# Optimization experiments

Measured on AMD Instinct MI355X. Metric: run time of the kernel, lower is better.

The kernel has to match this reference:

```python
import jax, jax.numpy as jnp
import numpy as np

T_STEPS, BATCH, DH, L = 256, 128, 512, 3  # L=3 is the only shape-consistent conv length (kernel=3, no pad)


def _conv3(x, W, b):
    # Conv1d(Dh->2, k=3) on a length-3 signal == full contraction over (Dh, 3)
    # x: (B, Dh, 3), W: (2, Dh, 3), b: (2,) -> (B, 2, 1)
    out = jnp.einsum('bdl,odl->bo', x, W) + b
    return out[:, :, None]


def setup_inputs() -> dict:
    key = jax.random.key(0)
    ks = jax.random.split(key, 5)
    inputs = jax.random.normal(ks[0], (T_STEPS, BATCH, DH, L), dtype=jnp.float32)
    h0 = jnp.zeros((BATCH, DH, L), jnp.float32)
    c0 = jnp.zeros((BATCH, DH, L), jnp.float32)
    scale = 1.0 / np.sqrt(DH * L).astype(np.float32)
    Wr = jax.random.normal(ks[1], (2, DH, L), jnp.float32) * scale  # recurrent_kernel (orthogonal-ish init)
    br = jnp.full((2,), 0.5, jnp.float32)                           # recurrent bias init 0.5
    Wc = jax.random.normal(ks[2], (2, DH, L), jnp.float32) * scale  # cell_memory_kernel
    bc = jnp.zeros((2,), jnp.float32)                               # cell_memory bias init 0
    Wi = jax.random.normal(ks[3], (2, DH, L), jnp.float32) * scale  # input_kernel
    bi = jax.random.normal(ks[4], (2,), jnp.float32) * scale
    return dict(inputs=inputs, h0=h0, c0=c0, Wr=Wr, br=br, Wc=Wc, bc=bc, Wi=Wi, bi=bi)


def reference(inputs, h0, c0, Wr, br, Wc, bc, Wi, bi):
    sig = jax.nn.sigmoid  # fun_gate

    def step(state, xt):
        h, c = state  # (B, Dh, 3) each
        cm = _conv3(c, Wc, bc)
        Cc, Ch = cm[:, 0:1], cm[:, 1:2]   # (B,1,1) each (chunk(2, dim=1))
        rm = _conv3(h, Wr, br)
        Hc, Hh = rm[:, 0:1], rm[:, 1:2]
        im = _conv3(xt, Wi, bi)
        Xc, Xh = im[:, 0:1], im[:, 1:2]
        gh = (1.0 - sig(Ch)) * Xh + (1.0 - sig(Hh)) * h   # broadcast (B,1,1)*(B,Dh,3)
        gc = (1.0 - sig(Hc)) * Xc + (1.0 - sig(Cc)) * c
        ht = jnp.tanh(gh)  # fun_main
        ct = jnp.tanh(gc)
        return (ht, ct), ht

    (hT, cT), outs = jax.lax.scan(step, (h0, c0), inputs)
    return outs, hT, cT
```

## Files before the change

kernel.cpp:

```cpp
#include <hip/hip_runtime.h>

#define T_STEPS 256
#define BATCH   128
#define FEAT    1536
#define NPAIRS  (T_STEPS * BATCH)

template <int CTRL, int RMASK>
__device__ __forceinline__ float dpp_add_step(float v) {
    int m = __builtin_amdgcn_update_dpp(0, __float_as_int(v), CTRL, RMASK, 0xF, true);
    return v + __int_as_float(m);
}

__device__ __forceinline__ float wave_reduce63(float v) {
    v = dpp_add_step<0x111, 0xF>(v);
    v = dpp_add_step<0x112, 0xF>(v);
    v = dpp_add_step<0x114, 0xF>(v);
    v = dpp_add_step<0x118, 0xF>(v);
    v = dpp_add_step<0x142, 0xA>(v);
    v = dpp_add_step<0x143, 0xC>(v);
    return v;
}

__device__ __forceinline__ float one_minus_sig(float x) {
    float e = __builtin_amdgcn_exp2f(x * 1.4426950408889634f);
    return __builtin_amdgcn_rcpf(1.0f + e);
}

__device__ __forceinline__ float tanh_fast(float x) {
    float e = __builtin_amdgcn_exp2f(x * 2.8853900817779268f);
    return fmaf(-2.0f, __builtin_amdgcn_rcpf(1.0f + e), 1.0f);
}

__device__ __forceinline__ void barrier_lds_only() {
    asm volatile("s_waitcnt lgkmcnt(0)\n\ts_barrier" ::: "memory");
}

__global__ __launch_bounds__(256) void xdot_kernel(
    const float* __restrict__ x,
    const float* __restrict__ Wi,
    const float* __restrict__ bi,
    float* __restrict__ X)
{
    const int p    = blockIdx.x;
    const int tid  = threadIdx.x;
    const int wid  = tid >> 6;
    const int lane = tid & 63;

    __shared__ float red[8];

    const float* xp = x + (size_t)p * FEAT;
    const float4 v4 = ((const float4*)xp)[tid];
    const float2 v2 = ((const float2*)(xp + 1024))[tid];

    const float4 w04 = ((const float4*)Wi)[tid];
    const float2 w02 = ((const float2*)(Wi + 1024))[tid];
    const float4 w14 = ((const float4*)(Wi + FEAT))[tid];
    const float2 w12 = ((const float2*)(Wi + FEAT + 1024))[tid];

    float a0 = v4.x * w04.x + v4.y * w04.y + v4.z * w04.z + v4.w * w04.w
             + v2.x * w02.x + v2.y * w02.y;
    float a1 = v4.x * w14.x + v4.y * w14.y + v4.z * w14.z + v4.w * w14.w
             + v2.x * w12.x + v2.y * w12.y;

    a0 = wave_reduce63(a0);
    a1 = wave_reduce63(a1);
    if (lane == 63) {
        red[wid * 2]     = a0;
        red[wid * 2 + 1] = a1;
    }
    __syncthreads();
    if (tid == 0) {
        const float s0 = red[0] + red[2] + red[4] + red[6] + bi[0];
        const float s1 = red[1] + red[3] + red[5] + red[7] + bi[1];
        const int b = p & (BATCH - 1);
        const int t = p >> 7;
        ((float2*)X)[b * T_STEPS + t] = make_float2(s0, s1);
    }
}

__global__ __launch_bounds__(256) void scan_kernel(
    const float* __restrict__ h0,
    const float* __restrict__ c0,
    const float* __restrict__ Wr, const float* __restrict__ br,
    const float* __restrict__ Wc, const float* __restrict__ bc,
    const float* __restrict__ X,
    float* __restrict__ outs,
    float* __restrict__ hT,
    float* __restrict__ cT)
{
    const int b    = blockIdx.x;
    const int tid  = threadIdx.x;
    const int wid  = tid >> 6;
    const int lane = tid & 63;

    __shared__ float4 red[2][4];
    __shared__ float2 Xsh[T_STEPS];

    Xsh[tid] = ((const float2*)X)[b * T_STEPS + tid];

    const float4 wr0_4 = ((const float4*)Wr)[tid];
    const float4 wr1_4 = ((const float4*)(Wr + FEAT))[tid];
    const float2 wr0_2 = ((const float2*)(Wr + 1024))[tid];
    const float2 wr1_2 = ((const float2*)(Wr + FEAT + 1024))[tid];
    const float4 wc0_4 = ((const float4*)Wc)[tid];
    const float4 wc1_4 = ((const float4*)(Wc + FEAT))[tid];
    const float2 wc0_2 = ((const float2*)(Wc + 1024))[tid];
    const float2 wc1_2 = ((const float2*)(Wc + FEAT + 1024))[tid];
    const float br0 = br[0], br1 = br[1];
    const float bc0 = bc[0], bc1 = bc[1];

    const float* h0b = h0 + (size_t)b * FEAT;
    const float* c0b = c0 + (size_t)b * FEAT;
    float4 h4 = ((const float4*)h0b)[tid];
    float2 h2 = ((const float2*)(h0b + 1024))[tid];
    float4 c4 = ((const float4*)c0b)[tid];
    float2 c2 = ((const float2*)(c0b + 1024))[tid];

    float* op = outs + (size_t)b * FEAT;
    const size_t OSTRIDE = (size_t)BATCH * FEAT;

    __syncthreads();

    auto step = [&](float4* buf, int t) {
        const float2 Xv = Xsh[t];

        float pHc = h4.x * wr0_4.x + h4.y * wr0_4.y + h4.z * wr0_4.z + h4.w * wr0_4.w
                  + h2.x * wr0_2.x + h2.y * wr0_2.y;
        float pHh = h4.x * wr1_4.x + h4.y * wr1_4.y + h4.z * wr1_4.z + h4.w * wr1_4.w
                  + h2.x * wr1_2.x + h2.y * wr1_2.y;
        float pCc = c4.x * wc0_4.x + c4.y * wc0_4.y + c4.z * wc0_4.z + c4.w * wc0_4.w
                  + c2.x * wc0_2.x + c2.y * wc0_2.y;
        float pCh = c4.x * wc1_4.x + c4.y * wc1_4.y + c4.z * wc1_4.z + c4.w * wc1_4.w
                  + c2.x * wc1_2.x + c2.y * wc1_2.y;

        pHc = wave_reduce63(pHc);
        pHh = wave_reduce63(pHh);
        pCc = wave_reduce63(pCc);
        pCh = wave_reduce63(pCh);

        if (lane == 63) {
            buf[wid] = make_float4(pHc, pHh, pCc, pCh);
        }
        barrier_lds_only();
        const float4 r0 = buf[0];
        const float4 r1 = buf[1];
        const float4 r2 = buf[2];
        const float4 r3 = buf[3];
        const float Hc = r0.x + r1.x + r2.x + r3.x + br0;
        const float Hh = r0.y + r1.y + r2.y + r3.y + br1;
        const float Cc = r0.z + r1.z + r2.z + r3.z + bc0;
        const float Ch = r0.w + r1.w + r2.w + r3.w + bc1;

        const float Ah = one_minus_sig(Ch) * Xv.y;
        const float Sh = one_minus_sig(Hh);
        const float Ac = one_minus_sig(Hc) * Xv.x;
        const float Sc = one_minus_sig(Cc);

        h4.x = tanh_fast(fmaf(Sh, h4.x, Ah));
        h4.y = tanh_fast(fmaf(Sh, h4.y, Ah));
        h4.z = tanh_fast(fmaf(Sh, h4.z, Ah));
        h4.w = tanh_fast(fmaf(Sh, h4.w, Ah));
        h2.x = tanh_fast(fmaf(Sh, h2.x, Ah));
        h2.y = tanh_fast(fmaf(Sh, h2.y, Ah));

        c4.x = tanh_fast(fmaf(Sc, c4.x, Ac));
        c4.y = tanh_fast(fmaf(Sc, c4.y, Ac));
        c4.z = tanh_fast(fmaf(Sc, c4.z, Ac));
        c4.w = tanh_fast(fmaf(Sc, c4.w, Ac));
        c2.x = tanh_fast(fmaf(Sc, c2.x, Ac));
        c2.y = tanh_fast(fmaf(Sc, c2.y, Ac));

        ((float4*)op)[tid]          = h4;
        ((float2*)(op + 1024))[tid] = h2;
        op += OSTRIDE;
    };

#pragma unroll 1
    for (int t = 0; t < T_STEPS; t += 2) {
        step(red[0], t);
        step(red[1], t + 1);
    }

    float* hp = hT + (size_t)b * FEAT;
    ((float4*)hp)[tid]          = h4;
    ((float2*)(hp + 1024))[tid] = h2;
    float* cp = cT + (size_t)b * FEAT;
    ((float4*)cp)[tid]          = c4;
    ((float2*)(cp + 1024))[tid] = c2;
}

extern "C" void kernel_launch(void* const* d_in, const int* in_sizes, int n_in,
                              void* d_out, int out_size, void* d_ws, size_t ws_size,
                              hipStream_t stream) {
    const float* inputs = (const float*)d_in[0];
    const float* h0     = (const float*)d_in[1];
    const float* c0     = (const float*)d_in[2];
    const float* Wr     = (const float*)d_in[3];
    const float* br     = (const float*)d_in[4];
    const float* Wc     = (const float*)d_in[5];
    const float* bc     = (const float*)d_in[6];
    const float* Wi     = (const float*)d_in[7];
    const float* bi     = (const float*)d_in[8];

    float* out = (float*)d_out;
    float* X   = (float*)d_ws;

    float* outs = out;
    float* hT   = out + (size_t)NPAIRS * FEAT;
    float* cT   = hT + (size_t)BATCH * FEAT;

    xdot_kernel<<<NPAIRS, 256, 0, stream>>>(inputs, Wi, bi, X);
    scan_kernel<<<BATCH, 256, 0, stream>>>(h0, c0, Wr, br, Wc, bc, X,
                                           outs, hT, cT);
}
```

Baseline: 449.8 us.

## Fuse input projection into scan kernel with two-step-ahead input prefetch

Measured after the change: 442.2 us. About the same (-1.7%).

```diff
diff --git a/kernel.cpp b/kernel.cpp
--- a/kernel.cpp
+++ b/kernel.cpp
@@ -35,55 +35,13 @@
     asm volatile("s_waitcnt lgkmcnt(0)\n\ts_barrier" ::: "memory");
 }
 
-__global__ __launch_bounds__(256) void xdot_kernel(
-    const float* __restrict__ x,
-    const float* __restrict__ Wi,
-    const float* __restrict__ bi,
-    float* __restrict__ X)
-{
-    const int p    = blockIdx.x;
-    const int tid  = threadIdx.x;
-    const int wid  = tid >> 6;
-    const int lane = tid & 63;
-
-    __shared__ float red[8];
-
-    const float* xp = x + (size_t)p * FEAT;
-    const float4 v4 = ((const float4*)xp)[tid];
-    const float2 v2 = ((const float2*)(xp + 1024))[tid];
-
-    const float4 w04 = ((const float4*)Wi)[tid];
-    const float2 w02 = ((const float2*)(Wi + 1024))[tid];
-    const float4 w14 = ((const float4*)(Wi + FEAT))[tid];
-    const float2 w12 = ((const float2*)(Wi + FEAT + 1024))[tid];
-
-    float a0 = v4.x * w04.x + v4.y * w04.y + v4.z * w04.z + v4.w * w04.w
-             + v2.x * w02.x + v2.y * w02.y;
-    float a1 = v4.x * w14.x + v4.y * w14.y + v4.z * w14.z + v4.w * w14.w
-             + v2.x * w12.x + v2.y * w12.y;
-
-    a0 = wave_reduce63(a0);
-    a1 = wave_reduce63(a1);
-    if (lane == 63) {
-        red[wid * 2]     = a0;
-        red[wid * 2 + 1] = a1;
-    }
-    __syncthreads();
-    if (tid == 0) {
-        const float s0 = red[0] + red[2] + red[4] + red[6] + bi[0];
-        const float s1 = red[1] + red[3] + red[5] + red[7] + bi[1];
-        const int b = p & (BATCH - 1);
-        const int t = p >> 7;
-        ((float2*)X)[b * T_STEPS + t] = make_float2(s0, s1);
-    }
-}
-
-__global__ __launch_bounds__(256) void scan_kernel(
+__global__ __launch_bounds__(256) void scan_fused_kernel(
+    const float* __restrict__ inputs,
     const float* __restrict__ h0,
     const float* __restrict__ c0,
     const float* __restrict__ Wr, const float* __restrict__ br,
     const float* __restrict__ Wc, const float* __restrict__ bc,
-    const float* __restrict__ X,
+    const float* __restrict__ Wi, const float* __restrict__ bi,
     float* __restrict__ outs,
     float* __restrict__ hT,
     float* __restrict__ cT)
@@ -93,10 +51,8 @@
     const int wid  = tid >> 6;
     const int lane = tid & 63;
 
-    __shared__ float4 red[2][4];
-    __shared__ float2 Xsh[T_STEPS];
-
-    Xsh[tid] = ((const float2*)X)[b * T_STEPS + tid];
+    __shared__ float4 red4[2][4];
+    __shared__ float2 red2[2][4];
 
     const float4 wr0_4 = ((const float4*)Wr)[tid];
     const float4 wr1_4 = ((const float4*)(Wr + FEAT))[tid];
@@ -106,8 +62,13 @@
     const float4 wc1_4 = ((const float4*)(Wc + FEAT))[tid];
     const float2 wc0_2 = ((const float2*)(Wc + 1024))[tid];
     const float2 wc1_2 = ((const float2*)(Wc + FEAT + 1024))[tid];
+    const float4 wi0_4 = ((const float4*)Wi)[tid];
+    const float4 wi1_4 = ((const float4*)(Wi + FEAT))[tid];
+    const float2 wi0_2 = ((const float2*)(Wi + 1024))[tid];
+    const float2 wi1_2 = ((const float2*)(Wi + FEAT + 1024))[tid];
     const float br0 = br[0], br1 = br[1];
     const float bc0 = bc[0], bc1 = bc[1];
+    const float bi0 = bi[0], bi1 = bi[1];
 
     const float* h0b = h0 + (size_t)b * FEAT;
     const float* c0b = c0 + (size_t)b * FEAT;
@@ -116,14 +77,18 @@
     float4 c4 = ((const float4*)c0b)[tid];
     float2 c2 = ((const float2*)(c0b + 1024))[tid];
 
+    const float*  xbase   = inputs + (size_t)b * FEAT;
+    const size_t  XSTRIDE = (size_t)BATCH * FEAT;
+
+    float4 xa4 = ((const float4*)xbase)[tid];
+    float2 xa2 = ((const float2*)(xbase + 1024))[tid];
+    float4 xb4 = ((const float4*)(xbase + XSTRIDE))[tid];
+    float2 xb2 = ((const float2*)(xbase + XSTRIDE + 1024))[tid];
+
     float* op = outs + (size_t)b * FEAT;
     const size_t OSTRIDE = (size_t)BATCH * FEAT;
 
-    __syncthreads();
-
-    auto step = [&](float4* buf, int t) {
-        const float2 Xv = Xsh[t];
-
+    auto step = [&](float4* buf4, float2* buf2, int t, float4& x4, float2& x2) {
         float pHc = h4.x * wr0_4.x + h4.y * wr0_4.y + h4.z * wr0_4.z + h4.w * wr0_4.w
                   + h2.x * wr0_2.x + h2.y * wr0_2.y;
         float pHh = h4.x * wr1_4.x + h4.y * wr1_4.y + h4.z * wr1_4.z + h4.w * wr1_4.w
@@ -132,28 +97,48 @@
                   + c2.x * wc0_2.x + c2.y * wc0_2.y;
         float pCh = c4.x * wc1_4.x + c4.y * wc1_4.y + c4.z * wc1_4.z + c4.w * wc1_4.w
                   + c2.x * wc1_2.x + c2.y * wc1_2.y;
+        float pXc = x4.x * wi0_4.x + x4.y * wi0_4.y + x4.z * wi0_4.z + x4.w * wi0_4.w
+                  + x2.x * wi0_2.x + x2.y * wi0_2.y;
+        float pXh = x4.x * wi1_4.x + x4.y * wi1_4.y + x4.z * wi1_4.z + x4.w * wi1_4.w
+                  + x2.x * wi1_2.x + x2.y * wi1_2.y;
+
+        {
+            const int tn = (t + 2 < T_STEPS) ? (t + 2) : (T_STEPS - 1);
+            const float* xp = xbase + (size_t)tn * XSTRIDE;
+            x4 = ((const float4*)xp)[tid];
+            x2 = ((const float2*)(xp + 1024))[tid];
+        }
 
         pHc = wave_reduce63(pHc);
         pHh = wave_reduce63(pHh);
         pCc = wave_reduce63(pCc);
         pCh = wave_reduce63(pCh);
+        pXc = wave_reduce63(pXc);
+        pXh = wave_reduce63(pXh);
 
         if (lane == 63) {
-            buf[wid] = make_float4(pHc, pHh, pCc, pCh);
+            buf4[wid] = make_float4(pHc, pHh, pCc, pCh);
+            buf2[wid] = make_float2(pXc, pXh);
         }
         barrier_lds_only();
-        const float4 r0 = buf[0];
-        const float4 r1 = buf[1];
-        const float4 r2 = buf[2];
-        const float4 r3 = buf[3];
+        const float4 r0 = buf4[0];
+        const float4 r1 = buf4[1];
+        const float4 r2 = buf4[2];
+        const float4 r3 = buf4[3];
+        const float2 s0 = buf2[0];
+        const float2 s1 = buf2[1];
+        const float2 s2 = buf2[2];
+        const float2 s3 = buf2[3];
         const float Hc = r0.x + r1.x + r2.x + r3.x + br0;
         const float Hh = r0.y + r1.y + r2.y + r3.y + br1;
         const float Cc = r0.z + r1.z + r2.z + r3.z + bc0;
         const float Ch = r0.w + r1.w + r2.w + r3.w + bc1;
+        const float Xc = s0.x + s1.x + s2.x + s3.x + bi0;
+        const float Xh = s0.y + s1.y + s2.y + s3.y + bi1;
 
-        const float Ah = one_minus_sig(Ch) * Xv.y;
+        const float Ah = one_minus_sig(Ch) * Xh;
         const float Sh = one_minus_sig(Hh);
-        const float Ac = one_minus_sig(Hc) * Xv.x;
+        const float Ac = one_minus_sig(Hc) * Xc;
         const float Sc = one_minus_sig(Cc);
 
         h4.x = tanh_fast(fmaf(Sh, h4.x, Ah));
@@ -177,8 +162,8 @@
 
 #pragma unroll 1
     for (int t = 0; t < T_STEPS; t += 2) {
-        step(red[0], t);
-        step(red[1], t + 1);
+        step(red4[0], red2[0], t,     xa4, xa2);
+        step(red4[1], red2[1], t + 1, xb4, xb2);
     }
 
     float* hp = hT + (size_t)b * FEAT;
@@ -202,14 +187,12 @@
     const float* Wi     = (const float*)d_in[7];
     const float* bi     = (const float*)d_in[8];
 
-    float* out = (float*)d_out;
-    float* X   = (float*)d_ws;
-
+    float* out  = (float*)d_out;
     float* outs = out;
     float* hT   = out + (size_t)NPAIRS * FEAT;
     float* cT   = hT + (size_t)BATCH * FEAT;
 
-    xdot_kernel<<<NPAIRS, 256, 0, stream>>>(inputs, Wi, bi, X);
-    scan_kernel<<<BATCH, 256, 0, stream>>>(h0, c0, Wr, br, Wc, bc, X,
-                                           outs, hT, cT);
+    scan_fused_kernel<<<BATCH, 256, 0, stream>>>(inputs, h0, c0, Wr, br,
+                                                 Wc, bc, Wi, bi,
+                                                 outs, hT, cT);
 }
```
